# Optimization experiments

Measured on AMD Instinct MI355X. Metric: run time of the kernel, lower is better.

## Reference

```python
import jax, jax.numpy as jnp
from jax import lax
import numpy as np

B = 131072   # batch
M = 16       # in_channel (message dim, m=2^k with k=4)
NCH = 8      # n_channel (complex symbols)
CD = 16      # 2*n_channel
TAPS = 3     # rayleigh channel taps
R = 0.5      # code rate k/n
EBNO = 10.0 ** (7.0 / 10.0)
EPS = 1e-5


def setup_inputs() -> dict:
    ks = jax.random.split(jax.random.key(0), 48)
    f32 = jnp.float32
    def lin(i, o, n):
        return jax.random.normal(ks[i], (o, n), f32) / np.float32(np.sqrt(n))
    def cw(i, o, c, k):
        return jax.random.normal(ks[i], (o, c, k), f32) / np.float32(np.sqrt(c * k))
    def bv(i, n):
        return 0.01 * jax.random.normal(ks[i], (n,), f32)
    return dict(
        x=jax.random.normal(ks[0], (B, M), f32),
        noise=jax.random.normal(ks[1], (B, CD), f32) / np.float32(np.sqrt(2 * R * EBNO)),
        fading=jax.random.normal(ks[2], (B, TAPS, 2), f32),
        ew1=lin(3, M, M), eb1=bv(4, M),
        ew2=lin(5, CD, M), eb2=bv(6, CD),
        ec1w=cw(7, NCH, 1, 2), ec1b=bv(8, NCH),
        ec2w=cw(9, NCH, NCH, 4), ec2b=bv(10, NCH),
        ec3w=cw(11, NCH, NCH, 2), ec3b=bv(12, NCH),
        ec4w=cw(13, NCH, NCH, 2), ec4b=bv(14, NCH),
        ew3=lin(15, CD, 2 * CD), eb3=bv(16, CD),
        bng=jnp.ones((CD,), f32), bnb=jnp.zeros((CD,), f32),
        pw1=lin(17, 2 * CD, CD), pb1=bv(18, 2 * CD),
        pw2=lin(19, 4 * CD, 2 * CD), pb2=bv(20, 4 * CD),
        pw3=lin(21, CD // 2, 4 * CD), pb3=bv(22, CD // 2),
        pw4=lin(23, 2, CD // 2), pb4=bv(24, 2),
        dw1=lin(25, CD, CD), db1=bv(26, CD),
        dc1w=cw(27, NCH, 1, 2), dc1b=bv(28, NCH),
        dc2w=cw(29, NCH, NCH, 4), dc2b=bv(30, NCH),
        dc3w=cw(31, NCH, NCH, 2), dc3b=bv(32, NCH),
        dc4w=cw(33, NCH, NCH, 2), dc4b=bv(34, NCH),
        dw2=lin(35, CD, 2 * CD), db2=bv(36, CD),
        dw3=lin(37, CD, CD), db3=bv(38, CD),
        dw4=lin(39, M, CD), db4=bv(40, M),
    )


def _conv(h, w, bias, s):
    y = lax.conv_general_dilated(h, w, (s,), 'VALID', dimension_numbers=('NCH', 'OIH', 'NCH'))
    return y + bias[None, :, None]


def reference(x, noise, fading, ew1, eb1, ew2, eb2, ec1w, ec1b, ec2w, ec2b, ec3w, ec3b,
              ec4w, ec4b, ew3, eb3, bng, bnb, pw1, pb1, pw2, pb2, pw3, pb3, pw4, pb4,
              dw1, db1, dc1w, dc1b, dc2w, dc2b, dc3w, dc3b, dc4w, dc4b, dw2, db2,
              dw3, db3, dw4, db4):
    elu, tanh = jax.nn.elu, jnp.tanh
    Bn = x.shape[0]
    # ---- encoder ----
    h = elu(x @ ew1.T + eb1)
    h = elu(h @ ew2.T + eb2)                       # (B, CD)
    h = h[:, None, :]                              # (B, 1, CD)
    h = tanh(_conv(h, ec1w, ec1b, 1))              # (B, NCH, 15)
    h = tanh(_conv(h, ec2w, ec2b, 2))              # (B, NCH, 6)
    h = tanh(_conv(h, ec3w, ec3b, 1))              # (B, NCH, 5)
    h = tanh(_conv(h, ec4w, ec4b, 1))              # (B, NCH, 4)
    h = h.reshape(Bn, 2 * bng.shape[0])            # (B, 2*CD)
    h = h @ ew3.T + eb3                            # (B, CD)
    mu = h.mean(0)
    var = h.var(0)                                 # biased var (torch BN training mode)
    enc = (h - mu) / jnp.sqrt(var + EPS) * bng + bnb
    # ---- rayleigh multipath channel: vectorized complex FIR over taps ----
    taps = fading.shape[1]
    xc = enc.reshape(Bn, -1, 2)                    # (B, NCH, 2) re/im pairs
    n_sym = xc.shape[1]
    pad = taps - 1
    padded = jnp.pad(xc, ((0, 0), (pad, pad), (0, 0)))
    idx = jnp.arange(n_sym + taps - 1)[:, None] + jnp.arange(taps)[None, :]
    win = padded[:, idx]                           # (B, L_out, taps, 2)
    ff = fading[:, ::-1]                           # per-example flipped taps
    yr = jnp.einsum('blt,bt->bl', win[..., 0], ff[..., 0]) - jnp.einsum('blt,bt->bl', win[..., 1], ff[..., 1])
    yi = jnp.einsum('blt,bt->bl', win[..., 0], ff[..., 1]) + jnp.einsum('blt,bt->bl', win[..., 1], ff[..., 0])
    y = jnp.stack([yr, yi], -1)[:, :n_sym]         # drop trailing taps-1 samples
    c = y.reshape(Bn, 2 * n_sym) + noise
    # ---- channel parameter estimation ----
    p = elu(c @ pw1.T + pb1)
    p = tanh(p @ pw2.T + pb2)
    p = tanh(p @ pw3.T + pb3)
    hp = p @ pw4.T + pb4                           # (B, 2) estimated complex h
    # ---- transform: complex division x / h ----
    cc = c.reshape(Bn, n_sym, 2)
    hr, hi = hp[:, 0:1], hp[:, 1:2]
    den = hr * hr + hi * hi
    tr = (cc[..., 0] * hr + cc[..., 1] * hi) / den
    ti = (cc[..., 1] * hr - cc[..., 0] * hi) / den
    t = jnp.stack([tr, ti], -1).reshape(Bn, 2 * n_sym)
    # ---- decoder ----
    d = tanh(t @ dw1.T + db1)
    d = d[:, None, :]
    d = tanh(_conv(d, dc1w, dc1b, 1))
    d = tanh(_conv(d, dc2w, dc2b, 2))
    d = tanh(_conv(d, dc3w, dc3b, 1))
    d = tanh(_conv(d, dc4w, dc4b, 1))
    d = d.reshape(Bn, -1)
    d = tanh(d @ dw2.T + db2)
    d = tanh(d @ dw3.T + db3)
    return d @ dw4.T + db4
```

## Files before the change

kernel.cpp:

```cpp
#include <hip/hip_runtime.h>


#define BTOT 131072
#define NT2  65536
#define BLK  128
#define NBLK 512
#define NW   6768

typedef float v2 __attribute__((ext_vector_type(2)));

constexpr int EW1 = 0;     constexpr int EB1 = 256;
constexpr int EW2 = 272;   constexpr int EB2 = 528;
constexpr int EC1W = 544;  constexpr int EC1B = 560;
constexpr int EC2W = 568;  constexpr int EC2B = 824;
constexpr int EC3W = 832;  constexpr int EC3B = 960;
constexpr int EC4W = 968;  constexpr int EC4B = 1096;
constexpr int EW3 = 1104;  constexpr int EB3 = 1616;
constexpr int BNG = 1632;  constexpr int BNB = 1648;
constexpr int PW1 = 1664;  constexpr int PB1 = 2176;
constexpr int PW2 = 2208;  constexpr int PB2 = 4256;
constexpr int PW3 = 4320;  constexpr int PB3 = 4832;
constexpr int PW4 = 4840;  constexpr int PB4 = 4856;
constexpr int DW1 = 4864;  constexpr int DB1 = 5120;
constexpr int DC1W = 5136; constexpr int DC1B = 5152;
constexpr int DC2W = 5160; constexpr int DC2B = 5416;
constexpr int DC3W = 5424; constexpr int DC3B = 5552;
constexpr int DC4W = 5560; constexpr int DC4B = 5688;
constexpr int DW2 = 5696;  constexpr int DB2 = 6208;
constexpr int DW3 = 6224;  constexpr int DB3 = 6480;
constexpr int DW4 = 6496;  constexpr int DB4 = 6752;

constexpr size_t WS_W    = 0;
constexpr size_t WS_SC   = 28672;
constexpr size_t WS_PART = 32768;
constexpr size_t WS_HENC = 131072;
constexpr size_t WS_NEED_HENC = WS_HENC + (size_t)BTOT * 16 * 4;

__device__ __forceinline__ v2 sp(float s) { v2 r; r.x = s; r.y = s; return r; }
__device__ __forceinline__ float bf2f(unsigned int u) {
  union { unsigned int i; float f; } v; v.i = u << 16; return v.f;
}
__device__ __forceinline__ unsigned short f2bf(float f) {
  union { float f; unsigned int i; } v; v.f = f;
  unsigned int x = v.i;
  return (unsigned short)((x + 0x7fffu + ((x >> 16) & 1u)) >> 16);
}
__device__ __forceinline__ void unpack8(uint4 u, float* f) {
  f[0] = bf2f(u.x & 0xffffu); f[1] = bf2f(u.x >> 16);
  f[2] = bf2f(u.y & 0xffffu); f[3] = bf2f(u.y >> 16);
  f[4] = bf2f(u.z & 0xffffu); f[5] = bf2f(u.z >> 16);
  f[6] = bf2f(u.w & 0xffffu); f[7] = bf2f(u.w >> 16);
}
__device__ __forceinline__ int sniff_bf16(const void* bng) {
  return *(const unsigned int*)bng != 0x3F800000u;
}
__device__ __forceinline__ void load16(const void* base, int b, int isbf, float* f) {
  if (isbf) {
    const uint4* p = (const uint4*)((const unsigned short*)base + (size_t)b * 16);
    unpack8(p[0], f); unpack8(p[1], f + 8);
  } else {
    const float4* p = (const float4*)((const float*)base + (size_t)b * 16);
#pragma unroll
    for (int q = 0; q < 4; q++) {
      float4 v = p[q];
      f[4 * q] = v.x; f[4 * q + 1] = v.y; f[4 * q + 2] = v.z; f[4 * q + 3] = v.w;
    }
  }
}
__device__ __forceinline__ void load16_2(const void* base, int bA, int bB, int isbf,
                                         v2* f) {
  float a[16], b[16];
  load16(base, bA, isbf, a);
  load16(base, bB, isbf, b);
#pragma unroll
  for (int j = 0; j < 16; j++) { f[j].x = a[j]; f[j].y = b[j]; }
}
__device__ __forceinline__ float tanh_f(float x) {
  float e = __expf(2.0f * x);
  return 1.0f - 2.0f * __builtin_amdgcn_rcpf(e + 1.0f);
}
__device__ __forceinline__ v2 tanh_v(v2 x) {
  v2 r; r.x = tanh_f(x.x); r.y = tanh_f(x.y); return r;
}
__device__ __forceinline__ v2 elu_v(v2 x) {
  v2 r;
  r.x = x.x > 0.0f ? x.x : __expf(x.x) - 1.0f;
  r.y = x.y > 0.0f ? x.y : __expf(x.y) - 1.0f;
  return r;
}

template <int OUT, int IN, int WOFF, int BOFF, int ACT>
__device__ __forceinline__ void dense2(const float* w, const v2* in, v2* out) {
#pragma unroll
  for (int m = 0; m < OUT; m++) {
    v2 v = sp(w[BOFF + m]);
#pragma unroll
    for (int k = 0; k < IN; k += 4) {
      float4 wv = *(const float4*)(w + WOFF + m * IN + k);
      v += in[k] * wv.x; v += in[k + 1] * wv.y;
      v += in[k + 2] * wv.z; v += in[k + 3] * wv.w;
    }
    if (ACT == 1) v = elu_v(v);
    if (ACT == 2) v = tanh_v(v);
    out[m] = v;
  }
}

template <int W1, int B1, int W2, int B2, int W3, int B3, int W4, int B4>
__device__ __forceinline__ void conv_chain2(const float* w, const v2 h[16],
                                            v2 flat[32]) {
  v2 c1[4][8];
  v2 c2[6][8];
#pragma unroll
  for (int p = 0; p < 6; p++) {
    const int p0 = (p == 0) ? 0 : (2 * p + 2);
#pragma unroll
    for (int pos = p0; pos <= 2 * p + 3; ++pos) {
#pragma unroll
      for (int o = 0; o < 8; o++) {
        float2 wv = *(const float2*)(w + W1 + o * 2);
        v2 v = h[pos] * wv.x + h[pos + 1] * wv.y + sp(w[B1 + o]);
        c1[pos & 3][o] = tanh_v(v);
      }
    }
#pragma unroll
    for (int o = 0; o < 8; o++) {
      v2 v = sp(w[B2 + o]);
#pragma unroll
      for (int i = 0; i < 8; i++) {
        float4 wv = *(const float4*)(w + W2 + (o * 8 + i) * 4);
        v += c1[(2 * p) & 3][i] * wv.x;
        v += c1[(2 * p + 1) & 3][i] * wv.y;
        v += c1[(2 * p + 2) & 3][i] * wv.z;
        v += c1[(2 * p + 3) & 3][i] * wv.w;
      }
      c2[p][o] = tanh_v(v);
    }
  }
  v2 c3[5][8];
#pragma unroll
  for (int p = 0; p < 5; p++) {
#pragma unroll
    for (int o = 0; o < 8; o++) {
      v2 v = sp(w[B3 + o]);
#pragma unroll
      for (int i = 0; i < 8; i++) {
        float2 wv = *(const float2*)(w + W3 + (o * 8 + i) * 2);
        v += c2[p][i] * wv.x + c2[p + 1][i] * wv.y;
      }
      c3[p][o] = tanh_v(v);
    }
  }
#pragma unroll
  for (int p = 0; p < 4; p++) {
#pragma unroll
    for (int o = 0; o < 8; o++) {
      v2 v = sp(w[B4 + o]);
#pragma unroll
      for (int i = 0; i < 8; i++) {
        float2 wv = *(const float2*)(w + W4 + (o * 8 + i) * 2);
        v += c3[p][i] * wv.x + c3[p + 1][i] * wv.y;
      }
      flat[o * 4 + p] = tanh_v(v);
    }
  }
}

__device__ __forceinline__ void encoder2(const void* __restrict__ x, int bA, int bB,
                                         int isbf, const float* w, v2 he[16]) {
  v2 xv[16];
  load16_2(x, bA, bB, isbf, xv);
  v2 h1[16], h2[16];
  dense2<16, 16, EW1, EB1, 1>(w, xv, h1);
  dense2<16, 16, EW2, EB2, 1>(w, h1, h2);
  v2 flat[32];
  conv_chain2<EC1W, EC1B, EC2W, EC2B, EC3W, EC3B, EC4W, EC4B>(w, h2, flat);
  dense2<16, 32, EW3, EB3, 0>(w, flat, he);
}

struct Segs {
  const void* src[40];
  int cnt[40];
  int off[40];
};
__global__ __launch_bounds__(256) void k_convert(Segs s, const void* __restrict__ bng_src,
                                                 float* __restrict__ dst) {
  const int isbf = sniff_bf16(bng_src);
  const int seg = blockIdx.x;
  const int n = s.cnt[seg];
  const int o = s.off[seg];
  if (isbf) {
    const unsigned short* p = (const unsigned short*)s.src[seg];
    for (int i = threadIdx.x; i < n; i += 256) dst[o + i] = bf2f((unsigned int)p[i]);
  } else {
    const float* p = (const float*)s.src[seg];
    for (int i = threadIdx.x; i < n; i += 256) dst[o + i] = p[i];
  }
}

__global__ __launch_bounds__(BLK, 1) void k_enc(const void* __restrict__ x,
                                                const void* __restrict__ bng_src,
                                                const float* __restrict__ wg,
                                                float* __restrict__ partials,
                                                float* __restrict__ henc,
                                                int store_henc) {
  __shared__ float sw[NW];
  for (int i = threadIdx.x; i < NW / 4; i += BLK)
    ((float4*)sw)[i] = ((const float4*)wg)[i];
  __syncthreads();

  const int isbf = sniff_bf16(bng_src);
  const int t = blockIdx.x * BLK + threadIdx.x;
  const int bA = t, bB = t + NT2;
  v2 he[16];
  encoder2(x, bA, bB, isbf, sw, he);

  if (store_henc) {
    float4* ha = (float4*)(henc + (size_t)bA * 16);
    float4* hb = (float4*)(henc + (size_t)bB * 16);
#pragma unroll
    for (int q = 0; q < 4; q++) {
      ha[q] = make_float4(he[4 * q].x, he[4 * q + 1].x, he[4 * q + 2].x, he[4 * q + 3].x);
      hb[q] = make_float4(he[4 * q].y, he[4 * q + 1].y, he[4 * q + 2].y, he[4 * q + 3].y);
    }
  }

  __shared__ float part[2][32];
  const int lane = threadIdx.x & 63;
  const int wid = threadIdx.x >> 6;
#pragma unroll
  for (int j = 0; j < 16; j++) {
    float s = he[j].x + he[j].y;
    float q = he[j].x * he[j].x + he[j].y * he[j].y;
#pragma unroll
    for (int m = 32; m >= 1; m >>= 1) {
      s += __shfl_xor(s, m, 64);
      q += __shfl_xor(q, m, 64);
    }
    if (lane == 0) { part[wid][j] = s; part[wid][16 + j] = q; }
  }
  __syncthreads();
  if (threadIdx.x < 32) {
    const int i = threadIdx.x;
    partials[blockIdx.x * 32 + i] = part[0][i] + part[1][i];
  }
}

__global__ __launch_bounds__(256) void k_red(const float* __restrict__ partials,
                                             const float* __restrict__ w,
                                             float* __restrict__ scsh) {
  __shared__ float red[8][32];
  __shared__ float tot[32];
  const int t = threadIdx.x;
  const int ch = t & 31, grp = t >> 5;
  float acc = 0.0f;
  for (int r = grp; r < NBLK; r += 8) acc += partials[r * 32 + ch];
  red[grp][ch] = acc;
  __syncthreads();
  if (t < 32) {
    float v = 0.0f;
#pragma unroll
    for (int g = 0; g < 8; g++) v += red[g][t];
    tot[t] = v;
  }
  __syncthreads();
  if (t < 16) {
    const float invB = 1.0f / (float)BTOT;
    float mu = tot[t] * invB;
    float var = tot[16 + t] * invB - mu * mu;
    float rstd = rsqrtf(var + 1e-5f);
    float sc = w[BNG + t] * rstd;
    scsh[t] = sc;
    scsh[16 + t] = w[BNB + t] - mu * sc;
  }
}

__global__ __launch_bounds__(BLK, 1) void k_main(const void* __restrict__ x,
                                                 const float* __restrict__ scsh,
                                                 const void* __restrict__ noise,
                                                 const void* __restrict__ fading,
                                                 const void* __restrict__ bng_src,
                                                 const float* __restrict__ wg,
                                                 const float* __restrict__ henc,
                                                 int use_henc,
                                                 void* __restrict__ out) {
  __shared__ float sw[NW];
  for (int i = threadIdx.x; i < NW / 4; i += BLK)
    ((float4*)sw)[i] = ((const float4*)wg)[i];
  __syncthreads();

  const int isbf = sniff_bf16(bng_src);
  const int t = blockIdx.x * BLK + threadIdx.x;
  const int bA = t, bB = t + NT2;
  v2 enc[16];
  if (use_henc) {
    const float4* pa = (const float4*)(henc + (size_t)bA * 16);
    const float4* pb = (const float4*)(henc + (size_t)bB * 16);
#pragma unroll
    for (int q = 0; q < 4; q++) {
      float4 a = pa[q], b = pb[q];
      enc[4 * q].x = a.x; enc[4 * q].y = b.x;
      enc[4 * q + 1].x = a.y; enc[4 * q + 1].y = b.y;
      enc[4 * q + 2].x = a.z; enc[4 * q + 2].y = b.z;
      enc[4 * q + 3].x = a.w; enc[4 * q + 3].y = b.w;
    }
  } else {
    encoder2(x, bA, bB, isbf, sw, enc);
  }
#pragma unroll
  for (int j = 0; j < 16; j++) enc[j] = enc[j] * scsh[j] + sp(scsh[16 + j]);

  v2 fr[3], fi[3];
  if (isbf) {
    const unsigned int* fa =
        (const unsigned int*)((const unsigned short*)fading + (size_t)bA * 6);
    const unsigned int* fb =
        (const unsigned int*)((const unsigned short*)fading + (size_t)bB * 6);
#pragma unroll
    for (int j = 0; j < 3; j++) {
      unsigned int ua = fa[j], ub = fb[j];
      fr[j].x = bf2f(ua & 0xffffu); fi[j].x = bf2f(ua >> 16);
      fr[j].y = bf2f(ub & 0xffffu); fi[j].y = bf2f(ub >> 16);
    }
  } else {
    const float2* fa = (const float2*)((const float*)fading + (size_t)bA * 6);
    const float2* fb = (const float2*)((const float*)fading + (size_t)bB * 6);
#pragma unroll
    for (int j = 0; j < 3; j++) {
      float2 a = fa[j], b = fb[j];
      fr[j].x = a.x; fi[j].x = a.y;
      fr[j].y = b.x; fi[j].y = b.y;
    }
  }
  v2 nz[16];
  load16_2(noise, bA, bB, isbf, nz);

  v2 c[16];
#pragma unroll
  for (int l = 0; l < 8; l++) {
    v2 ar = sp(0.0f), ai = sp(0.0f);
#pragma unroll
    for (int j = 0; j < 3; j++) {
      if (l - j >= 0) {
        v2 xr = enc[2 * (l - j)], xi = enc[2 * (l - j) + 1];
        ar += xr * fr[j] - xi * fi[j];
        ai += xr * fi[j] + xi * fr[j];
      }
    }
    c[2 * l] = ar + nz[2 * l];
    c[2 * l + 1] = ai + nz[2 * l + 1];
  }
  v2 p1[32];
  dense2<32, 16, PW1, PB1, 1>(sw, c, p1);
  v2 p3[8];
#pragma unroll
  for (int j = 0; j < 8; j++) p3[j] = sp(sw[PB3 + j]);
#pragma unroll
  for (int n0 = 0; n0 < 64; n0 += 4) {
    v2 tv[4];
#pragma unroll
    for (int u = 0; u < 4; u++) {
      const int n = n0 + u;
      v2 v = sp(sw[PB2 + n]);
#pragma unroll
      for (int k = 0; k < 32; k += 4) {
        float4 wv = *(const float4*)(sw + PW2 + n * 32 + k);
        v += p1[k] * wv.x; v += p1[k + 1] * wv.y;
        v += p1[k + 2] * wv.z; v += p1[k + 3] * wv.w;
      }
      tv[u] = tanh_v(v);
    }
#pragma unroll
    for (int j = 0; j < 8; j++) {
      float4 wv = *(const float4*)(sw + PW3 + j * 64 + n0);
      p3[j] += tv[0] * wv.x + tv[1] * wv.y + tv[2] * wv.z + tv[3] * wv.w;
    }
  }
#pragma unroll
  for (int j = 0; j < 8; j++) p3[j] = tanh_v(p3[j]);
  v2 hr = sp(sw[PB4 + 0]), hi = sp(sw[PB4 + 1]);
#pragma unroll
  for (int k = 0; k < 8; k++) {
    hr += p3[k] * sw[PW4 + k];
    hi += p3[k] * sw[PW4 + 8 + k];
  }
  v2 den = hr * hr + hi * hi;
  v2 inv; inv.x = __builtin_amdgcn_rcpf(den.x); inv.y = __builtin_amdgcn_rcpf(den.y);
  v2 tt[16];
#pragma unroll
  for (int l = 0; l < 8; l++) {
    v2 c0 = c[2 * l], c1v = c[2 * l + 1];
    tt[2 * l] = (c0 * hr + c1v * hi) * inv;
    tt[2 * l + 1] = (c1v * hr - c0 * hi) * inv;
  }
  v2 d1[16];
  dense2<16, 16, DW1, DB1, 2>(sw, tt, d1);
  v2 flat[32];
  conv_chain2<DC1W, DC1B, DC2W, DC2B, DC3W, DC3B, DC4W, DC4B>(sw, d1, flat);
  v2 d2[16], d3[16], o[16];
  dense2<16, 32, DW2, DB2, 2>(sw, flat, d2);
  dense2<16, 16, DW3, DB3, 2>(sw, d2, d3);
  dense2<16, 16, DW4, DB4, 0>(sw, d3, o);

  if (isbf) {
    unsigned int ovA[8], ovB[8];
#pragma unroll
    for (int j = 0; j < 8; j++) {
      ovA[j] = (unsigned int)f2bf(o[2 * j].x) | ((unsigned int)f2bf(o[2 * j + 1].x) << 16);
      ovB[j] = (unsigned int)f2bf(o[2 * j].y) | ((unsigned int)f2bf(o[2 * j + 1].y) << 16);
    }
    uint4* oa = (uint4*)((unsigned short*)out + (size_t)bA * 16);
    uint4* ob = (uint4*)((unsigned short*)out + (size_t)bB * 16);
    oa[0] = make_uint4(ovA[0], ovA[1], ovA[2], ovA[3]);
    oa[1] = make_uint4(ovA[4], ovA[5], ovA[6], ovA[7]);
    ob[0] = make_uint4(ovB[0], ovB[1], ovB[2], ovB[3]);
    ob[1] = make_uint4(ovB[4], ovB[5], ovB[6], ovB[7]);
  } else {
    float4* oa = (float4*)((float*)out + (size_t)bA * 16);
    float4* ob = (float4*)((float*)out + (size_t)bB * 16);
#pragma unroll
    for (int q = 0; q < 4; q++) {
      oa[q] = make_float4(o[4 * q].x, o[4 * q + 1].x, o[4 * q + 2].x, o[4 * q + 3].x);
      ob[q] = make_float4(o[4 * q].y, o[4 * q + 1].y, o[4 * q + 2].y, o[4 * q + 3].y);
    }
  }
}

extern "C" void kernel_launch(void* const* d_in, const int* in_sizes, int n_in,
                              void* d_out, int out_size, void* d_ws, size_t ws_size,
                              hipStream_t stream) {
  float* wbuf = (float*)((char*)d_ws + WS_W);
  float* scsh = (float*)((char*)d_ws + WS_SC);
  float* partials = (float*)((char*)d_ws + WS_PART);
  float* henc = (float*)((char*)d_ws + WS_HENC);
  const int use_henc = (ws_size >= WS_NEED_HENC) ? 1 : 0;

  static const int offs[40] = {
      EW1, EB1, EW2, EB2, EC1W, EC1B, EC2W, EC2B, EC3W, EC3B, EC4W, EC4B,
      EW3, EB3, BNG, BNB, PW1, PB1, PW2, PB2, PW3, PB3, PW4, PB4,
      DW1, DB1, DC1W, DC1B, DC2W, DC2B, DC3W, DC3B, DC4W, DC4B,
      DW2, DB2, DW3, DB3, DW4, DB4};
  Segs segs;
  for (int k = 0; k < 40; k++) {
    segs.src[k] = d_in[3 + k];
    segs.cnt[k] = in_sizes[3 + k];
    segs.off[k] = offs[k];
  }
  const void* bng_src = d_in[17];
  k_convert<<<40, 256, 0, stream>>>(segs, bng_src, wbuf);
  k_enc<<<NBLK, BLK, 0, stream>>>(d_in[0], bng_src, wbuf, partials, henc, use_henc);
  k_red<<<1, 256, 0, stream>>>(partials, wbuf, scsh);
  k_main<<<NBLK, BLK, 0, stream>>>(d_in[0], scsh, d_in[1], d_in[2], bng_src, wbuf,
                                   henc, use_henc, d_out);
}
```

Before: 258.4 us.

## Fuse convert, encoder, BN reduction and main into one grid-synced kernel

```diff
diff --git a/kernel.cpp b/kernel.cpp
--- a/kernel.cpp
+++ b/kernel.cpp
@@ -30,11 +30,9 @@
 constexpr int DW3 = 6224;  constexpr int DB3 = 6480;
 constexpr int DW4 = 6496;  constexpr int DB4 = 6752;
 
-constexpr size_t WS_W    = 0;
-constexpr size_t WS_SC   = 28672;
+constexpr size_t WS_SC   = 0;
+constexpr size_t WS_SYNC = 256;
 constexpr size_t WS_PART = 32768;
-constexpr size_t WS_HENC = 131072;
-constexpr size_t WS_NEED_HENC = WS_HENC + (size_t)BTOT * 16 * 4;
 
 __device__ __forceinline__ v2 sp(float s) { v2 r; r.x = s; r.y = s; return r; }
 __device__ __forceinline__ float bf2f(unsigned int u) {
@@ -166,149 +164,120 @@
   }
 }
 
-__device__ __forceinline__ void encoder2(const void* __restrict__ x, int bA, int bB,
-                                         int isbf, const float* w, v2 he[16]) {
-  v2 xv[16];
-  load16_2(x, bA, bB, isbf, xv);
-  v2 h1[16], h2[16];
-  dense2<16, 16, EW1, EB1, 1>(w, xv, h1);
-  dense2<16, 16, EW2, EB2, 1>(w, h1, h2);
-  v2 flat[32];
-  conv_chain2<EC1W, EC1B, EC2W, EC2B, EC3W, EC3B, EC4W, EC4B>(w, h2, flat);
-  dense2<16, 32, EW3, EB3, 0>(w, flat, he);
-}
-
 struct Segs {
   const void* src[40];
   int cnt[40];
   int off[40];
 };
-__global__ __launch_bounds__(256) void k_convert(Segs s, const void* __restrict__ bng_src,
-                                                 float* __restrict__ dst) {
+
+__global__ __launch_bounds__(BLK, 2) void k_fused(
+    const void* __restrict__ x, const void* __restrict__ noise,
+    const void* __restrict__ fading, const void* __restrict__ bng_src,
+    Segs segs, float* __restrict__ scsh, float* __restrict__ partials,
+    unsigned int* __restrict__ sync, void* __restrict__ out) {
   const int isbf = sniff_bf16(bng_src);
-  const int seg = blockIdx.x;
-  const int n = s.cnt[seg];
-  const int o = s.off[seg];
+
+  __shared__ float sw[NW];
   if (isbf) {
-    const unsigned short* p = (const unsigned short*)s.src[seg];
-    for (int i = threadIdx.x; i < n; i += 256) dst[o + i] = bf2f((unsigned int)p[i]);
+    for (int s = 0; s < 40; s++) {
+      const unsigned short* p = (const unsigned short*)segs.src[s];
+      const int n = segs.cnt[s], o = segs.off[s];
+      for (int i = threadIdx.x; i < n; i += BLK) sw[o + i] = bf2f((unsigned int)p[i]);
+    }
   } else {
-    const float* p = (const float*)s.src[seg];
-    for (int i = threadIdx.x; i < n; i += 256) dst[o + i] = p[i];
-  }
-}
-
-__global__ __launch_bounds__(BLK, 1) void k_enc(const void* __restrict__ x,
-                                                const void* __restrict__ bng_src,
-                                                const float* __restrict__ wg,
-                                                float* __restrict__ partials,
-                                                float* __restrict__ henc,
-                                                int store_henc) {
-  __shared__ float sw[NW];
-  for (int i = threadIdx.x; i < NW / 4; i += BLK)
-    ((float4*)sw)[i] = ((const float4*)wg)[i];
+    for (int s = 0; s < 40; s++) {
+      const float* p = (const float*)segs.src[s];
+      const int n = segs.cnt[s], o = segs.off[s];
+      for (int i = threadIdx.x; i < n; i += BLK) sw[o + i] = p[i];
+    }
+  }
   __syncthreads();
 
-  const int isbf = sniff_bf16(bng_src);
   const int t = blockIdx.x * BLK + threadIdx.x;
   const int bA = t, bB = t + NT2;
   v2 he[16];
-  encoder2(x, bA, bB, isbf, sw, he);
-
-  if (store_henc) {
-    float4* ha = (float4*)(henc + (size_t)bA * 16);
-    float4* hb = (float4*)(henc + (size_t)bB * 16);
-#pragma unroll
-    for (int q = 0; q < 4; q++) {
-      ha[q] = make_float4(he[4 * q].x, he[4 * q + 1].x, he[4 * q + 2].x, he[4 * q + 3].x);
-      hb[q] = make_float4(he[4 * q].y, he[4 * q + 1].y, he[4 * q + 2].y, he[4 * q + 3].y);
-    }
-  }
-
+  {
+    v2 xv[16];
+    load16_2(x, bA, bB, isbf, xv);
+    v2 h1[16], h2[16];
+    dense2<16, 16, EW1, EB1, 1>(sw, xv, h1);
+    dense2<16, 16, EW2, EB2, 1>(sw, h1, h2);
+    v2 flat[32];
+    conv_chain2<EC1W, EC1B, EC2W, EC2B, EC3W, EC3B, EC4W, EC4B>(sw, h2, flat);
+    dense2<16, 32, EW3, EB3, 0>(sw, flat, he);
+  }
   __shared__ float part[2][32];
-  const int lane = threadIdx.x & 63;
-  const int wid = threadIdx.x >> 6;
-#pragma unroll
-  for (int j = 0; j < 16; j++) {
-    float s = he[j].x + he[j].y;
-    float q = he[j].x * he[j].x + he[j].y * he[j].y;
-#pragma unroll
-    for (int m = 32; m >= 1; m >>= 1) {
-      s += __shfl_xor(s, m, 64);
-      q += __shfl_xor(q, m, 64);
-    }
-    if (lane == 0) { part[wid][j] = s; part[wid][16 + j] = q; }
+  {
+    const int lane = threadIdx.x & 63;
+    const int wid = threadIdx.x >> 6;
+#pragma unroll
+    for (int j = 0; j < 16; j++) {
+      float s = he[j].x + he[j].y;
+      float q = he[j].x * he[j].x + he[j].y * he[j].y;
+#pragma unroll
+      for (int m = 32; m >= 1; m >>= 1) {
+        s += __shfl_xor(s, m, 64);
+        q += __shfl_xor(q, m, 64);
+      }
+      if (lane == 0) { part[wid][j] = s; part[wid][16 + j] = q; }
+    }
   }
   __syncthreads();
-  if (threadIdx.x < 32) {
-    const int i = threadIdx.x;
-    partials[blockIdx.x * 32 + i] = part[0][i] + part[1][i];
-  }
-}
-
-__global__ __launch_bounds__(256) void k_red(const float* __restrict__ partials,
-                                             const float* __restrict__ w,
-                                             float* __restrict__ scsh) {
-  __shared__ float red[8][32];
-  __shared__ float tot[32];
-  const int t = threadIdx.x;
-  const int ch = t & 31, grp = t >> 5;
-  float acc = 0.0f;
-  for (int r = grp; r < NBLK; r += 8) acc += partials[r * 32 + ch];
-  red[grp][ch] = acc;
+  if (threadIdx.x < 32)
+    partials[blockIdx.x * 32 + threadIdx.x] = part[0][threadIdx.x] + part[1][threadIdx.x];
+
+  __shared__ int is_last;
+  if (threadIdx.x == 0) {
+    __threadfence();
+    unsigned int old = atomicAdd(&sync[0], 1u);
+    is_last = (old == NBLK - 1) ? 1 : 0;
+  }
   __syncthreads();
-  if (t < 32) {
-    float v = 0.0f;
-#pragma unroll
-    for (int g = 0; g < 8; g++) v += red[g][t];
-    tot[t] = v;
-  }
-  __syncthreads();
-  if (t < 16) {
-    const float invB = 1.0f / (float)BTOT;
-    float mu = tot[t] * invB;
-    float var = tot[16 + t] * invB - mu * mu;
-    float rstd = rsqrtf(var + 1e-5f);
-    float sc = w[BNG + t] * rstd;
-    scsh[t] = sc;
-    scsh[16 + t] = w[BNB + t] - mu * sc;
-  }
-}
-
-__global__ __launch_bounds__(BLK, 1) void k_main(const void* __restrict__ x,
-                                                 const float* __restrict__ scsh,
-                                                 const void* __restrict__ noise,
-                                                 const void* __restrict__ fading,
-                                                 const void* __restrict__ bng_src,
-                                                 const float* __restrict__ wg,
-                                                 const float* __restrict__ henc,
-                                                 int use_henc,
-                                                 void* __restrict__ out) {
-  __shared__ float sw[NW];
-  for (int i = threadIdx.x; i < NW / 4; i += BLK)
-    ((float4*)sw)[i] = ((const float4*)wg)[i];
-  __syncthreads();
-
-  const int isbf = sniff_bf16(bng_src);
-  const int t = blockIdx.x * BLK + threadIdx.x;
-  const int bA = t, bB = t + NT2;
+  if (is_last) {
+    __shared__ float red[4][32];
+    const int ch = threadIdx.x & 31, grp = threadIdx.x >> 5;
+    float acc = 0.0f;
+    for (int r = grp; r < NBLK; r += 4) acc += partials[r * 32 + ch];
+    red[grp][ch] = acc;
+    __syncthreads();
+    if (threadIdx.x < 32) {
+      float v = red[0][threadIdx.x] + red[1][threadIdx.x] + red[2][threadIdx.x] +
+                red[3][threadIdx.x];
+      if (threadIdx.x < 16) {
+        red[0][threadIdx.x] = v;
+      } else {
+        red[1][threadIdx.x - 16] = v;
+      }
+    }
+    __syncthreads();
+    if (threadIdx.x < 16) {
+      const float invB = 1.0f / (float)BTOT;
+      float mu = red[0][threadIdx.x] * invB;
+      float var = red[1][threadIdx.x] * invB - mu * mu;
+      float rstd = rsqrtf(var + 1e-5f);
+      float sc = sw[BNG + threadIdx.x] * rstd;
+      scsh[threadIdx.x] = sc;
+      scsh[16 + threadIdx.x] = sw[BNB + threadIdx.x] - mu * sc;
+    }
+    __syncthreads();
+    if (threadIdx.x == 0) {
+      __threadfence();
+      __hip_atomic_store(&sync[1], 1u, __ATOMIC_RELEASE, __HIP_MEMORY_SCOPE_AGENT);
+    }
+  } else {
+    if (threadIdx.x == 0) {
+      while (__hip_atomic_load(&sync[1], __ATOMIC_ACQUIRE,
+                               __HIP_MEMORY_SCOPE_AGENT) == 0) {
+        __builtin_amdgcn_s_sleep(2);
+      }
+    }
+    __syncthreads();
+    __threadfence();
+  }
+
   v2 enc[16];
-  if (use_henc) {
-    const float4* pa = (const float4*)(henc + (size_t)bA * 16);
-    const float4* pb = (const float4*)(henc + (size_t)bB * 16);
-#pragma unroll
-    for (int q = 0; q < 4; q++) {
-      float4 a = pa[q], b = pb[q];
-      enc[4 * q].x = a.x; enc[4 * q].y = b.x;
-      enc[4 * q + 1].x = a.y; enc[4 * q + 1].y = b.y;
-      enc[4 * q + 2].x = a.z; enc[4 * q + 2].y = b.z;
-      enc[4 * q + 3].x = a.w; enc[4 * q + 3].y = b.w;
-    }
-  } else {
-    encoder2(x, bA, bB, isbf, sw, enc);
-  }
-#pragma unroll
-  for (int j = 0; j < 16; j++) enc[j] = enc[j] * scsh[j] + sp(scsh[16 + j]);
+#pragma unroll
+  for (int j = 0; j < 16; j++) enc[j] = he[j] * scsh[j] + sp(scsh[16 + j]);
 
   v2 fr[3], fi[3];
   if (isbf) {
@@ -429,11 +398,9 @@
 extern "C" void kernel_launch(void* const* d_in, const int* in_sizes, int n_in,
                               void* d_out, int out_size, void* d_ws, size_t ws_size,
                               hipStream_t stream) {
-  float* wbuf = (float*)((char*)d_ws + WS_W);
   float* scsh = (float*)((char*)d_ws + WS_SC);
+  unsigned int* sync = (unsigned int*)((char*)d_ws + WS_SYNC);
   float* partials = (float*)((char*)d_ws + WS_PART);
-  float* henc = (float*)((char*)d_ws + WS_HENC);
-  const int use_henc = (ws_size >= WS_NEED_HENC) ? 1 : 0;
 
   static const int offs[40] = {
       EW1, EB1, EW2, EB2, EC1W, EC1B, EC2W, EC2B, EC3W, EC3B, EC4W, EC4B,
@@ -447,9 +414,8 @@
     segs.off[k] = offs[k];
   }
   const void* bng_src = d_in[17];
-  k_convert<<<40, 256, 0, stream>>>(segs, bng_src, wbuf);
-  k_enc<<<NBLK, BLK, 0, stream>>>(d_in[0], bng_src, wbuf, partials, henc, use_henc);
-  k_red<<<1, 256, 0, stream>>>(partials, wbuf, scsh);
-  k_main<<<NBLK, BLK, 0, stream>>>(d_in[0], scsh, d_in[1], d_in[2], bng_src, wbuf,
-                                   henc, use_henc, d_out);
-}
+
+  hipMemsetAsync(sync, 0, 8, stream);
+  k_fused<<<NBLK, BLK, 0, stream>>>(d_in[0], d_in[1], d_in[2], bng_src, segs,
+                                    scsh, partials, sync, d_out);
+}
```

Measured after the change: 901.0 us. 3.49x slower.
